# Performance work log

Measured on AMD Instinct MI355X. Metric: run time of the kernel, lower is better.

## Reference

```python
import jax, jax.numpy as jnp
import numpy as np

EPS = 1e-6
NUM_HEADS = 16


def _layernorm(x, g, b):
    m = jnp.mean(x, axis=-1, keepdims=True)
    v = jnp.mean(jnp.square(x - m), axis=-1, keepdims=True)
    return (x - m) / jnp.sqrt(v + EPS) * g + b


def _rotate_half(x):
    x1, x2 = jnp.split(x, 2, axis=-1)
    return jnp.concatenate([-x2, x1], axis=-1)


def setup_inputs() -> dict:
    key = jax.random.key(0)
    B, N, C = 2, 2048, 1024
    H = NUM_HEADS
    D = C // H
    F = int(C * 4.0)
    ks = jax.random.split(key, 12)
    s = 0.02
    pos = jnp.arange(N)[:, None].astype(jnp.float32)
    inv_freq = 1.0 / (10000.0 ** (jnp.arange(0, D, 2, dtype=jnp.float32) / D))
    freqs = pos * inv_freq[None, :]          # [N, D/2]
    emb = jnp.concatenate([freqs, freqs], axis=-1)  # [N, D]
    return {
        "x": jax.random.normal(ks[0], (B, N, C), jnp.float32),
        "rotary_cos": jnp.cos(emb),
        "rotary_sin": jnp.sin(emb),
        "ln1_g": jnp.ones((C,), jnp.float32),
        "ln1_b": jnp.zeros((C,), jnp.float32),
        "Wq": jax.random.normal(ks[1], (C, C), jnp.float32) * s,
        "bq": jnp.zeros((C,), jnp.float32),
        "Wk": jax.random.normal(ks[2], (C, C), jnp.float32) * s,
        "bk": jnp.zeros((C,), jnp.float32),
        "Wv": jax.random.normal(ks[3], (C, C), jnp.float32) * s,
        "bv": jnp.zeros((C,), jnp.float32),
        "Wo": jax.random.normal(ks[4], (C, C), jnp.float32) * s,
        "bo": jnp.zeros((C,), jnp.float32),
        "ln2_g": jnp.ones((C,), jnp.float32),
        "ln2_b": jnp.zeros((C,), jnp.float32),
        "W1": jax.random.normal(ks[5], (F, C), jnp.float32) * s,
        "b1": jnp.zeros((F,), jnp.float32),
        "W2": jax.random.normal(ks[6], (C, F), jnp.float32) * s,
        "b2": jnp.zeros((C,), jnp.float32),
    }


def reference(x, rotary_cos, rotary_sin, ln1_g, ln1_b, Wq, bq, Wk, bk, Wv, bv,
              Wo, bo, ln2_g, ln2_b, W1, b1, W2, b2):
    B, N, C = x.shape
    H = NUM_HEADS
    D = C // H

    # --- attention branch ---
    h = _layernorm(x, ln1_g, ln1_b)
    q = (h @ Wq.T + bq).reshape(B, N, H, D).transpose(0, 2, 1, 3)  # [B,H,N,D]
    k = (h @ Wk.T + bk).reshape(B, N, H, D).transpose(0, 2, 1, 3)
    v = (h @ Wv.T + bv).reshape(B, N, H, D).transpose(0, 2, 1, 3)

    cos = rotary_cos[None, None, :, :]  # [1,1,N,D]
    sin = rotary_sin[None, None, :, :]
    q = q * cos + _rotate_half(q) * sin
    k = k * cos + _rotate_half(k) * sin

    scale = D ** -0.5
    attn = jnp.einsum('bhnd,bhmd->bhnm', q, k) * scale
    attn = jax.nn.softmax(attn, axis=-1)
    out = jnp.einsum('bhnm,bhmd->bhnd', attn, v)
    out = out.transpose(0, 2, 1, 3).reshape(B, N, C)
    out = out @ Wo.T + bo
    x = x + out

    # --- MLP branch ---
    h = _layernorm(x, ln2_g, ln2_b)
    h = jax.nn.gelu(h @ W1.T + b1, approximate=False)  # torch nn.GELU exact
    h = h @ W2.T + b2
    return x + h
```

## Files before the change

### kernel.cpp

```cpp
#include <hip/hip_runtime.h>
#include <hip/hip_bf16.h>

#define B_ 2
#define N_ 2048
#define C_ 1024
#define H_ 16
#define D_ 64
#define F_ 4096
#define M_ 4096

typedef __attribute__((ext_vector_type(8))) short bf16x8;
typedef __attribute__((ext_vector_type(4))) float f32x4;

__device__ inline unsigned short f2bf(float f) {
  unsigned int u = __float_as_uint(f);
  u = (u + 0x7FFFu + ((u >> 16) & 1u)) >> 16;
  return (unsigned short)u;
}

__global__ __launch_bounds__(256)
void cvt_all(const float4* __restrict__ s0, const float4* __restrict__ s1,
             const float4* __restrict__ s2, const float4* __restrict__ s3,
             const float4* __restrict__ s4, const float4* __restrict__ s5,
             ushort4* __restrict__ d0, ushort4* __restrict__ d1,
             ushort4* __restrict__ d2, ushort4* __restrict__ d3,
             ushort4* __restrict__ d4, ushort4* __restrict__ d5) {
  int b = blockIdx.x;
  const float4* s; ushort4* d; int i;
  if      (b < 1024) { s = s0; d = d0; i = b * 256 + threadIdx.x; }
  else if (b < 2048) { s = s1; d = d1; i = (b - 1024) * 256 + threadIdx.x; }
  else if (b < 3072) { s = s2; d = d2; i = (b - 2048) * 256 + threadIdx.x; }
  else if (b < 4096) { s = s3; d = d3; i = (b - 3072) * 256 + threadIdx.x; }
  else if (b < 8192) { s = s4; d = d4; i = (b - 4096) * 256 + threadIdx.x; }
  else               { s = s5; d = d5; i = (b - 8192) * 256 + threadIdx.x; }
  float4 f = s[i];
  ushort4 o;
  o.x = f2bf(f.x); o.y = f2bf(f.y); o.z = f2bf(f.z); o.w = f2bf(f.w);
  d[i] = o;
}

__global__ __launch_bounds__(256)
void ln_kernel(const float* __restrict__ x, const float* __restrict__ g,
               const float* __restrict__ b, unsigned short* __restrict__ out) {
  __shared__ float red[8];
  const int row = blockIdx.x;
  const int t = threadIdx.x;
  const float4 xv = *(const float4*)(x + row * 1024 + t * 4);
  float s  = xv.x + xv.y + xv.z + xv.w;
  float sq = xv.x * xv.x + xv.y * xv.y + xv.z * xv.z + xv.w * xv.w;
  #pragma unroll
  for (int off = 32; off >= 1; off >>= 1) {
    s  += __shfl_down(s, off);
    sq += __shfl_down(sq, off);
  }
  const int lane = t & 63, wave = t >> 6;
  if (lane == 0) { red[wave * 2] = s; red[wave * 2 + 1] = sq; }
  __syncthreads();
  float ts = red[0] + red[2] + red[4] + red[6];
  float tq = red[1] + red[3] + red[5] + red[7];
  float mean = ts * (1.0f / 1024.0f);
  float var  = tq * (1.0f / 1024.0f) - mean * mean;
  float rstd = rsqrtf(var + 1e-6f);
  float xs[4] = {xv.x, xv.y, xv.z, xv.w};
  #pragma unroll
  for (int i = 0; i < 4; i++) {
    int c = t * 4 + i;
    float y = (xs[i] - mean) * rstd * g[c] + b[c];
    out[row * 1024 + c] = f2bf(y);
  }
}

template<int MODE, int BN>
__global__ __launch_bounds__(256)
void gemm_bt(const unsigned short* __restrict__ A,
             const unsigned short* __restrict__ Bw,
             int K, int Nout, int npc,
             const float* __restrict__ bias,
             const float* __restrict__ resid,
             unsigned short* __restrict__ out_bf,
             float* __restrict__ out_f32) {
  constexpr int NJ = BN / 32;
  __shared__ unsigned short sA[2][128 * 64];
  __shared__ unsigned short sB[2][BN * 64];
  const int t = threadIdx.x;
  const int wave = t >> 6, lane = t & 63;
  const int quad = lane >> 4, l16 = lane & 15;
  const int wm = (wave & 1) * 64, wn = (wave >> 1) * (BN / 2);
  const int id = blockIdx.y * gridDim.x + blockIdx.x;
  const int xcd = id & 7, r_ = id >> 3;
  const int m_blk = xcd * 4 + (r_ & 3);
  const int n_blk = r_ >> 2;
  const int m0 = m_blk * 128, n0 = n_blk * BN;

  f32x4 acc[4][NJ];
  #pragma unroll
  for (int i = 0; i < 4; i++)
    #pragma unroll
    for (int j = 0; j < NJ; j++) acc[i][j] = (f32x4){0.f, 0.f, 0.f, 0.f};

  const int sc = (((t & 7) ^ ((t >> 3) & 7)) * 8);
  const unsigned short* gA = A  + (m0 + (t >> 3)) * K + sc;
  const unsigned short* gB = Bw + (n0 + (t >> 3)) * K + sc;

  auto stage = [&](int k0, int buf) {
    unsigned short* lA = &sA[buf][(wave * 8) * 64];
    unsigned short* lB = &sB[buf][(wave * 8) * 64];
    #pragma unroll
    for (int i = 0; i < 4; i++)
      __builtin_amdgcn_global_load_lds((const unsigned int*)(gA + (32 * i) * K + k0),
                                       (unsigned int*)(lA + 32 * i * 64), 16, 0, 0);
    #pragma unroll
    for (int i = 0; i < BN / 32; i++)
      __builtin_amdgcn_global_load_lds((const unsigned int*)(gB + (32 * i) * K + k0),
                                       (unsigned int*)(lB + 32 * i * 64), 16, 0, 0);
  };

  stage(0, 0);
  __syncthreads();

  const int so0 = ((quad ^ (l16 & 7)) * 8);
  const int so1 = (((4 + quad) ^ (l16 & 7)) * 8);

  const int nk = K >> 6;
  for (int kt = 0; kt < nk; kt++) {
    const int cur = kt & 1;
    if (kt + 1 < nk) stage((kt + 1) * 64, cur ^ 1);
    #pragma unroll
    for (int kk = 0; kk < 2; kk++) {
      const int so = kk ? so1 : so0;
      bf16x8 af[4], bfr[NJ];
      #pragma unroll
      for (int i = 0; i < 4; i++)
        af[i] = *(const bf16x8*)(&sA[cur][(wm + i * 16 + l16) * 64 + so]);
      #pragma unroll
      for (int j = 0; j < NJ; j++)
        bfr[j] = *(const bf16x8*)(&sB[cur][(wn + j * 16 + l16) * 64 + so]);
      #pragma unroll
      for (int i = 0; i < 4; i++)
        #pragma unroll
        for (int j = 0; j < NJ; j++)
          acc[i][j] = __builtin_amdgcn_mfma_f32_16x16x32_bf16(af[i], bfr[j], acc[i][j], 0, 0, 0);
    }
    __syncthreads();
  }

  #pragma unroll
  for (int i = 0; i < 4; i++) {
    #pragma unroll
    for (int j = 0; j < NJ; j++) {
      int col = n0 + wn + j * 16 + l16;
      #pragma unroll
      for (int r = 0; r < 4; r++) {
        int row = m0 + wm + i * 16 + quad * 4 + r;
        float v = acc[i][j][r];
        if (MODE == 1 || MODE == 3) {
          out_f32[row * Nout + col] = v + bias[col] + resid[row * Nout + col];
        } else {
          v += bias[col];
          float w = v * (1.0f + 0.044715f * v * v);
          float gl = v / (1.0f + __expf(-1.5957691216f * w));
          out_bf[row * Nout + col] = f2bf(gl);
        }
      }
    }
  }
}

template<int EPI>
__global__ __launch_bounds__(512, 1)
void gemm256(const unsigned short* __restrict__ A,
             const unsigned short* __restrict__ Bw,
             const float* __restrict__ bias,
             const float* __restrict__ bq, const float* __restrict__ bk,
             const float* __restrict__ bv,
             const float* __restrict__ rc, const float* __restrict__ rs,
             unsigned short* __restrict__ o0,
             unsigned short* __restrict__ ko, unsigned short* __restrict__ vt) {
  const int K = 1024;
  __shared__ unsigned short sA[2][256 * 64];
  __shared__ unsigned short sB[2][256 * 64];
  const int t = threadIdx.x;
  const int wave = t >> 6, lane = t & 63;
  const int quad = lane >> 4, l16 = lane & 15;
  const int wm = (wave & 1) * 128, wn = (wave >> 1) * 64;
  const int id = blockIdx.x;
  const int xcd = id & 7, r_ = id >> 3;
  int m_blk, n_blk;
  if (EPI == 0) { n_blk = xcd * 2 + (r_ >> 4); m_blk = r_ & 15; }
  else          { m_blk = xcd * 2 + r_ / 12;   n_blk = r_ % 12; }
  const int m0 = m_blk * 256, n0 = n_blk * 256;

  f32x4 acc[8][4];
  #pragma unroll
  for (int i = 0; i < 8; i++)
    #pragma unroll
    for (int j = 0; j < 4; j++) acc[i][j] = (f32x4){0.f, 0.f, 0.f, 0.f};

  const int sc = (((t & 7) ^ ((t >> 3) & 7)) * 8);
  const unsigned short* gA = A  + (m0 + (t >> 3)) * K + sc;
  const unsigned short* gB = Bw + (n0 + (t >> 3)) * K + sc;

  auto stage_pair = [&](int k0, int buf, int pr) {
    if (pr < 2) {
      unsigned short* lA = &sA[buf][(wave * 8) * 64];
      #pragma unroll
      for (int r = pr * 2; r < pr * 2 + 2; r++)
        __builtin_amdgcn_global_load_lds((const unsigned int*)(gA + (64 * r) * K + k0),
                                         (unsigned int*)(lA + 64 * r * 64), 16, 0, 0);
    } else {
      unsigned short* lB = &sB[buf][(wave * 8) * 64];
      #pragma unroll
      for (int r = (pr - 2) * 2; r < (pr - 2) * 2 + 2; r++)
        __builtin_amdgcn_global_load_lds((const unsigned int*)(gB + (64 * r) * K + k0),
                                         (unsigned int*)(lB + 64 * r * 64), 16, 0, 0);
    }
  };

  stage_pair(0, 0, 0); stage_pair(0, 0, 1); stage_pair(0, 0, 2); stage_pair(0, 0, 3);
  stage_pair(64, 1, 0);
  asm volatile("s_waitcnt vmcnt(2)" ::: "memory");
  __builtin_amdgcn_s_barrier();

  const int so0 = ((quad ^ (l16 & 7)) * 8);
  const int so1 = (((4 + quad) ^ (l16 & 7)) * 8);

  const int nk = K >> 6;
  for (int t_ = 0; t_ < nk; t_++) {
    const int R = t_ & 1;
    const unsigned short* rA = sA[R];
    const unsigned short* rB = sB[R];
    #pragma unroll
    for (int p = 0; p < 4; p++) {
      const int kk = p >> 1, ih = p & 1;
      const int so = kk ? so1 : so0;
      bf16x8 af[4], bfr[4];
      #pragma unroll
      for (int ii = 0; ii < 4; ii++)
        af[ii] = *(const bf16x8*)(&rA[(wm + (ih * 4 + ii) * 16 + l16) * 64 + so]);
      #pragma unroll
      for (int j = 0; j < 4; j++)
        bfr[j] = *(const bf16x8*)(&rB[(wn + j * 16 + l16) * 64 + so]);
      if (p < 3 && t_ + 1 < nk) stage_pair((t_ + 1) * 64, R ^ 1, p + 1);
      __builtin_amdgcn_s_barrier();
      asm volatile("s_waitcnt lgkmcnt(0)" ::: "memory");
      __builtin_amdgcn_sched_barrier(0);
      __builtin_amdgcn_s_setprio(1);
      #pragma unroll
      for (int ii = 0; ii < 4; ii++)
        #pragma unroll
        for (int j = 0; j < 4; j++)
          acc[ih * 4 + ii][j] =
              __builtin_amdgcn_mfma_f32_16x16x32_bf16(af[ii], bfr[j], acc[ih * 4 + ii][j], 0, 0, 0);
      __builtin_amdgcn_s_setprio(0);
      if (p < 3) __builtin_amdgcn_s_barrier();
    }
    __builtin_amdgcn_s_barrier();
    if (t_ + 2 < nk) {
      stage_pair((t_ + 2) * 64, R, 0);
      asm volatile("s_waitcnt vmcnt(2)" ::: "memory");
      __builtin_amdgcn_s_barrier();
    } else if (t_ + 1 < nk) {
      asm volatile("s_waitcnt vmcnt(0)" ::: "memory");
      __builtin_amdgcn_s_barrier();
    }
  }

  if (EPI == 0) {
    #pragma unroll
    for (int i = 0; i < 8; i++) {
      #pragma unroll
      for (int j = 0; j < 4; j++) {
        int col = n0 + wn + j * 16 + l16;
        float bb = bias[col];
        #pragma unroll
        for (int r = 0; r < 4; r++) {
          int row = m0 + wm + i * 16 + quad * 4 + r;
          float v = acc[i][j][r] + bb;
          float w = v * (1.0f + 0.044715f * v * v);
          float gl = v / (1.0f + __expf(-1.5957691216f * w));
          o0[row * 4096 + col] = f2bf(gl);
        }
      }
    }
  } else {
    const int rgn = n_blk >> 2;
    const int c0 = (n_blk & 3) * 256;
    if (rgn == 2) {
      #pragma unroll
      for (int i = 0; i < 8; i++) {
        int row0 = m0 + wm + i * 16 + quad * 4;
        int bidx = row0 >> 11, n0r = row0 & 2047;
        #pragma unroll
        for (int j = 0; j < 4; j++) {
          int d = j * 16 + l16;
          int c = c0 + wn + d;
          int h = c >> 6;
          float bb = bv[c];
          __hip_bfloat162 p01 = __float22bfloat162_rn(float2{acc[i][j][0] + bb, acc[i][j][1] + bb});
          __hip_bfloat162 p23 = __float22bfloat162_rn(float2{acc[i][j][2] + bb, acc[i][j][3] + bb});
          unsigned int u01, u23;
          __builtin_memcpy(&u01, &p01, 4);
          __builtin_memcpy(&u23, &p23, 4);
          *(uint2*)(vt + (((bidx * 16 + h) * 64) + d) * 2048 + n0r) = make_uint2(u01, u23);
        }
      }
    } else {
      const float* bia = (rgn == 0) ? bq : bk;
      unsigned short* outp = (rgn == 0) ? o0 : ko;
      #pragma unroll
      for (int i = 0; i < 8; i++) {
        #pragma unroll
        for (int r = 0; r < 4; r++) {
          int row = m0 + wm + i * 16 + quad * 4 + r;
          int bidx = row >> 11, n = row & 2047;
          #pragma unroll
          for (int j = 0; j < 4; j++) {
            int d = j * 16 + l16;
            int c = c0 + wn + d;
            int h = c >> 6;
            int oi = ((bidx * 16 + h) * 2048 + n) * 64 + d;
            float val = acc[i][j][r] + bia[c];
            float pv  = acc[i][j ^ 2][r] + bia[c ^ 32];
            float rot = (j < 2) ? -pv : pv;
            float y = val * rc[n * 64 + d] + rot * rs[n * 64 + d];
            if (rgn == 0) y *= 0.125f;
            outp[oi] = f2bf(y);
          }
        }
      }
    }
  }
}

__global__ __launch_bounds__(256)
void flash_attn(const unsigned short* __restrict__ q,
                const unsigned short* __restrict__ k,
                const unsigned short* __restrict__ vt,
                unsigned short* __restrict__ o) {
  __shared__ unsigned short sK[2][64 * 64];
  __shared__ unsigned short sVt[2][64 * 64];
  __shared__ unsigned short sPt[2][4][16 * 72];
  const int t = threadIdx.x;
  const int wave = t >> 6, lane = t & 63;
  const int quad = lane >> 4, l16 = lane & 15;
  const int id = blockIdx.y * gridDim.x + blockIdx.x;
  const int bh = (id & 7) * 4 + ((id >> 3) & 3);
  const int qb = id >> 5;
  const int base = bh * (N_ * D_);

  bf16x8 qa[2][2];
  #pragma unroll
  for (int qt = 0; qt < 2; qt++) {
    int qrow = qb * 128 + wave * 32 + qt * 16 + l16;
    #pragma unroll
    for (int kk = 0; kk < 2; kk++)
      qa[qt][kk] = *(const bf16x8*)(q + base + qrow * D_ + kk * 32 + quad * 8);
  }
  float l_i[2] = {0.f, 0.f};
  f32x4 o_acc[2][4];
  #pragma unroll
  for (int qt = 0; qt < 2; qt++)
    #pragma unroll
    for (int dt = 0; dt < 4; dt++) o_acc[qt][dt] = (f32x4){0.f, 0.f, 0.f, 0.f};

  const int sc = (((t & 7) ^ ((t >> 3) & 7)) * 8);
  const unsigned short* gK  = k  + base + (t >> 3) * 64 + sc;
  const unsigned short* gVt = vt + bh * (64 * 2048) + (t >> 3) * 2048 + sc;

  auto stage = [&](int kt, int buf) {
    unsigned short* lK = &sK[buf][(wave * 8) * 64];
    unsigned short* lV = &sVt[buf][(wave * 8) * 64];
    #pragma unroll
    for (int i = 0; i < 2; i++) {
      __builtin_amdgcn_global_load_lds((const unsigned int*)(gK + (kt * 64 + 32 * i) * 64),
                                       (unsigned int*)(lK + 32 * i * 64), 16, 0, 0);
      __builtin_amdgcn_global_load_lds((const unsigned int*)(gVt + 32 * i * 2048 + kt * 64),
                                       (unsigned int*)(lV + 32 * i * 64), 16, 0, 0);
    }
  };
  stage(0, 0);
  __syncthreads();

  const int so0 = ((quad ^ (l16 & 7)) * 8);
  const int so1 = (((4 + quad) ^ (l16 & 7)) * 8);

  for (int kt = 0; kt < N_ / 64; kt++) {
    const int cur = kt & 1;
    if (kt < N_ / 64 - 1) stage(kt + 1, cur ^ 1);

    f32x4 s_acc[2][4];
    #pragma unroll
    for (int nt = 0; nt < 4; nt++) {
      bf16x8 kb0 = *(const bf16x8*)(&sK[cur][(nt * 16 + l16) * 64 + so0]);
      bf16x8 kb1 = *(const bf16x8*)(&sK[cur][(nt * 16 + l16) * 64 + so1]);
      #pragma unroll
      for (int qt = 0; qt < 2; qt++) {
        f32x4 a = (f32x4){0.f, 0.f, 0.f, 0.f};
        a = __builtin_amdgcn_mfma_f32_16x16x32_bf16(kb0, qa[qt][0], a, 0, 0, 0);
        a = __builtin_amdgcn_mfma_f32_16x16x32_bf16(kb1, qa[qt][1], a, 0, 0, 0);
        s_acc[qt][nt] = a;
      }
    }
    #pragma unroll
    for (int qt = 0; qt < 2; qt++) {
      float rsum = 0.f;
      #pragma unroll
      for (int nt = 0; nt < 4; nt++)
        #pragma unroll
        for (int r = 0; r < 4; r++) {
          float p = __expf(s_acc[qt][nt][r]);
          s_acc[qt][nt][r] = p;
          rsum += p;
        }
      rsum += __shfl_xor(rsum, 16);
      rsum += __shfl_xor(rsum, 32);
      l_i[qt] += rsum;
      #pragma unroll
      for (int nt = 0; nt < 4; nt++) {
        __hip_bfloat162 p01 = __float22bfloat162_rn(float2{s_acc[qt][nt][0], s_acc[qt][nt][1]});
        __hip_bfloat162 p23 = __float22bfloat162_rn(float2{s_acc[qt][nt][2], s_acc[qt][nt][3]});
        unsigned int u01, u23;
        __builtin_memcpy(&u01, &p01, 4);
        __builtin_memcpy(&u23, &p23, 4);
        *(uint2*)(&sPt[qt][wave][l16 * 72 + nt * 16 + quad * 4]) = make_uint2(u01, u23);
      }
    }
    __asm__ volatile("s_waitcnt lgkmcnt(0)" ::: "memory");
    bf16x8 pt[2][2];
    #pragma unroll
    for (int qt = 0; qt < 2; qt++) {
      pt[qt][0] = *(const bf16x8*)(&sPt[qt][wave][l16 * 72 + quad * 8]);
      pt[qt][1] = *(const bf16x8*)(&sPt[qt][wave][l16 * 72 + 32 + quad * 8]);
    }
    #pragma unroll
    for (int dt = 0; dt < 4; dt++) {
      int d0 = dt * 16 + l16;
      bf16x8 va0 = *(const bf16x8*)(&sVt[cur][d0 * 64 + so0]);
      bf16x8 va1 = *(const bf16x8*)(&sVt[cur][d0 * 64 + so1]);
      #pragma unroll
      for (int qt = 0; qt < 2; qt++) {
        o_acc[qt][dt] = __builtin_amdgcn_mfma_f32_16x16x32_bf16(va0, pt[qt][0], o_acc[qt][dt], 0, 0, 0);
        o_acc[qt][dt] = __builtin_amdgcn_mfma_f32_16x16x32_bf16(va1, pt[qt][1], o_acc[qt][dt], 0, 0, 0);
      }
    }
    __syncthreads();
  }

  const int b = bh >> 4, h = bh & 15;
  #pragma unroll
  for (int qt = 0; qt < 2; qt++) {
    const float inv = 1.0f / l_i[qt];
    const int tok = b * N_ + qb * 128 + wave * 32 + qt * 16 + l16;
    #pragma unroll
    for (int dt = 0; dt < 4; dt++) {
      __hip_bfloat162 p01 = __float22bfloat162_rn(float2{o_acc[qt][dt][0] * inv, o_acc[qt][dt][1] * inv});
      __hip_bfloat162 p23 = __float22bfloat162_rn(float2{o_acc[qt][dt][2] * inv, o_acc[qt][dt][3] * inv});
      unsigned int u01, u23;
      __builtin_memcpy(&u01, &p01, 4);
      __builtin_memcpy(&u23, &p23, 4);
      int col = h * 64 + dt * 16 + quad * 4;
      *(uint2*)(o + tok * C_ + col) = make_uint2(u01, u23);
    }
  }
}

extern "C" void kernel_launch(void* const* d_in, const int* in_sizes, int n_in,
                              void* d_out, int out_size, void* d_ws, size_t ws_size,
                              hipStream_t stream) {
  const float* x   = (const float*)d_in[0];
  const float* rc  = (const float*)d_in[1];
  const float* rs  = (const float*)d_in[2];
  const float* g1  = (const float*)d_in[3];
  const float* be1 = (const float*)d_in[4];
  const float* Wq  = (const float*)d_in[5];
  const float* bq  = (const float*)d_in[6];
  const float* Wk  = (const float*)d_in[7];
  const float* bk  = (const float*)d_in[8];
  const float* Wv  = (const float*)d_in[9];
  const float* bv  = (const float*)d_in[10];
  const float* Wo  = (const float*)d_in[11];
  const float* bo  = (const float*)d_in[12];
  const float* g2  = (const float*)d_in[13];
  const float* be2 = (const float*)d_in[14];
  const float* W1  = (const float*)d_in[15];
  const float* b1m = (const float*)d_in[16];
  const float* W2  = (const float*)d_in[17];
  const float* b2m = (const float*)d_in[18];
  float* out = (float*)d_out;

  char* ws = (char*)d_ws;
  unsigned short* wqkv = (unsigned short*)(ws + 0);
  unsigned short* wo   = (unsigned short*)(ws + 6291456);
  unsigned short* w1   = (unsigned short*)(ws + 8388608);
  unsigned short* w2   = (unsigned short*)(ws + 16777216);
  unsigned short* h1   = (unsigned short*)(ws + 25165824);
  unsigned short* qa   = (unsigned short*)(ws + 33554432);
  unsigned short* ka   = (unsigned short*)(ws + 41943040);
  unsigned short* va   = (unsigned short*)(ws + 50331648);
  unsigned short* ao   = (unsigned short*)(ws + 58720256);
  float*          x1   = (float*)(ws + 67108864);
  unsigned short* u    = (unsigned short*)(ws + 33554432);

  cvt_all<<<12288, 256, 0, stream>>>(
      (const float4*)Wq, (const float4*)Wk, (const float4*)Wv, (const float4*)Wo,
      (const float4*)W1, (const float4*)W2,
      (ushort4*)wqkv, (ushort4*)(wqkv + 1048576), (ushort4*)(wqkv + 2097152),
      (ushort4*)wo, (ushort4*)w1, (ushort4*)w2);

  ln_kernel<<<4096, 256, 0, stream>>>(x, g1, be1, h1);
  gemm256<1><<<192, 512, 0, stream>>>(h1, wqkv, nullptr, bq, bk, bv, rc, rs, qa, ka, va);
  flash_attn<<<dim3(16, 32), 256, 0, stream>>>(qa, ka, va, ao);
  gemm_bt<1, 64><<<dim3(16, 32), 256, 0, stream>>>(ao, wo, 1024, 1024, 2, bo, x, nullptr, x1);
  ln_kernel<<<4096, 256, 0, stream>>>(x1, g2, be2, h1);
  gemm256<0><<<256, 512, 0, stream>>>(h1, w1, b1m, nullptr, nullptr, nullptr, nullptr, nullptr,
                                      u, nullptr, nullptr);
  gemm_bt<3, 64><<<dim3(16, 32), 256, 0, stream>>>(u, w2, 4096, 1024, 2, b2m, x1, nullptr, out);
}
```

Baseline: 373.9 us.

## Split flash attention over KV halves with 512-thread blocks and a combine kernel

Flash attention now splits the key/value sequence into two halves, each handled by a separate block of 512 threads covering 256 query rows. Each block writes an unnormalized bf16 partial output and its row sums, and a new attn_norm kernel adds the halves and divides by the total sum. The aim is more parallelism and shorter per-block loops, at the cost of an extra kernel launch and extra partial-output traffic. Partials are rounded to bf16 before combining, which adds some rounding error. The merge is only exact because the softmax is apparently computed without a running max, so both halves share the same implicit scale.

Measured after the change: 375.6 us. Within noise of the previous version (+0.4%).

```diff
diff --git a/kernel.cpp b/kernel.cpp
--- a/kernel.cpp
+++ b/kernel.cpp
@@ -16,6 +16,10 @@
   unsigned int u = __float_as_uint(f);
   u = (u + 0x7FFFu + ((u >> 16) & 1u)) >> 16;
   return (unsigned short)u;
+}
+__device__ inline float bf2f(unsigned short u) {
+  unsigned int x = ((unsigned int)u) << 16;
+  return __uint_as_float(x);
 }
 
 __global__ __launch_bounds__(256)
@@ -332,26 +336,29 @@
   }
 }
 
-__global__ __launch_bounds__(256)
+__global__ __launch_bounds__(512)
 void flash_attn(const unsigned short* __restrict__ q,
                 const unsigned short* __restrict__ k,
                 const unsigned short* __restrict__ vt,
-                unsigned short* __restrict__ o) {
+                unsigned short* __restrict__ o0h,
+                unsigned short* __restrict__ o1h,
+                float* __restrict__ l0g, float* __restrict__ l1g) {
   __shared__ unsigned short sK[2][64 * 64];
   __shared__ unsigned short sVt[2][64 * 64];
-  __shared__ unsigned short sPt[2][4][16 * 72];
+  __shared__ unsigned short sPt[2][8][16 * 72];
   const int t = threadIdx.x;
   const int wave = t >> 6, lane = t & 63;
   const int quad = lane >> 4, l16 = lane & 15;
-  const int id = blockIdx.y * gridDim.x + blockIdx.x;
+  const int id = blockIdx.x;
   const int bh = (id & 7) * 4 + ((id >> 3) & 3);
-  const int qb = id >> 5;
+  const int qb = (id >> 5) & 7;
+  const int kvh = id >> 8;
   const int base = bh * (N_ * D_);
 
   bf16x8 qa[2][2];
   #pragma unroll
   for (int qt = 0; qt < 2; qt++) {
-    int qrow = qb * 128 + wave * 32 + qt * 16 + l16;
+    int qrow = qb * 256 + wave * 32 + qt * 16 + l16;
     #pragma unroll
     for (int kk = 0; kk < 2; kk++)
       qa[qt][kk] = *(const bf16x8*)(q + base + qrow * D_ + kk * 32 + quad * 8);
@@ -368,25 +375,21 @@
   const unsigned short* gVt = vt + bh * (64 * 2048) + (t >> 3) * 2048 + sc;
 
   auto stage = [&](int kt, int buf) {
-    unsigned short* lK = &sK[buf][(wave * 8) * 64];
-    unsigned short* lV = &sVt[buf][(wave * 8) * 64];
-    #pragma unroll
-    for (int i = 0; i < 2; i++) {
-      __builtin_amdgcn_global_load_lds((const unsigned int*)(gK + (kt * 64 + 32 * i) * 64),
-                                       (unsigned int*)(lK + 32 * i * 64), 16, 0, 0);
-      __builtin_amdgcn_global_load_lds((const unsigned int*)(gVt + 32 * i * 2048 + kt * 64),
-                                       (unsigned int*)(lV + 32 * i * 64), 16, 0, 0);
-    }
+    __builtin_amdgcn_global_load_lds((const unsigned int*)(gK + kt * 64 * 64),
+                                     (unsigned int*)(&sK[buf][(wave * 8) * 64]), 16, 0, 0);
+    __builtin_amdgcn_global_load_lds((const unsigned int*)(gVt + kt * 64),
+                                     (unsigned int*)(&sVt[buf][(wave * 8) * 64]), 16, 0, 0);
   };
-  stage(0, 0);
+  const int kt0 = kvh * 16, kt1 = kt0 + 16;
+  stage(kt0, 0);
   __syncthreads();
 
   const int so0 = ((quad ^ (l16 & 7)) * 8);
   const int so1 = (((4 + quad) ^ (l16 & 7)) * 8);
 
-  for (int kt = 0; kt < N_ / 64; kt++) {
+  for (int kt = kt0; kt < kt1; kt++) {
     const int cur = kt & 1;
-    if (kt < N_ / 64 - 1) stage(kt + 1, cur ^ 1);
+    if (kt + 1 < kt1) stage(kt + 1, cur ^ 1);
 
     f32x4 s_acc[2][4];
     #pragma unroll
@@ -446,22 +449,53 @@
     __syncthreads();
   }
 
+  unsigned short* op = kvh ? o1h : o0h;
+  float* lp = kvh ? l1g : l0g;
   const int b = bh >> 4, h = bh & 15;
   #pragma unroll
   for (int qt = 0; qt < 2; qt++) {
-    const float inv = 1.0f / l_i[qt];
-    const int tok = b * N_ + qb * 128 + wave * 32 + qt * 16 + l16;
+    const int qrow = qb * 256 + wave * 32 + qt * 16 + l16;
+    if (quad == 0) lp[bh * 2048 + qrow] = l_i[qt];
+    const int tok = b * N_ + qrow;
     #pragma unroll
     for (int dt = 0; dt < 4; dt++) {
-      __hip_bfloat162 p01 = __float22bfloat162_rn(float2{o_acc[qt][dt][0] * inv, o_acc[qt][dt][1] * inv});
-      __hip_bfloat162 p23 = __float22bfloat162_rn(float2{o_acc[qt][dt][2] * inv, o_acc[qt][dt][3] * inv});
+      __hip_bfloat162 p01 = __float22bfloat162_rn(float2{o_acc[qt][dt][0], o_acc[qt][dt][1]});
+      __hip_bfloat162 p23 = __float22bfloat162_rn(float2{o_acc[qt][dt][2], o_acc[qt][dt][3]});
       unsigned int u01, u23;
       __builtin_memcpy(&u01, &p01, 4);
       __builtin_memcpy(&u23, &p23, 4);
       int col = h * 64 + dt * 16 + quad * 4;
-      *(uint2*)(o + tok * C_ + col) = make_uint2(u01, u23);
-    }
-  }
+      *(uint2*)(op + tok * C_ + col) = make_uint2(u01, u23);
+    }
+  }
+}
+
+__global__ __launch_bounds__(256)
+void attn_norm(const unsigned short* __restrict__ o0h,
+               const unsigned short* __restrict__ o1h,
+               const float* __restrict__ l0g, const float* __restrict__ l1g,
+               unsigned short* __restrict__ o) {
+  const int i = (blockIdx.x * 256 + threadIdx.x) * 8;
+  const int row = i >> 10, c = i & 1023;
+  const int h = c >> 6;
+  const int b = row >> 11, n = row & 2047;
+  const int li = (b * 16 + h) * 2048 + n;
+  const float inv = 1.0f / (l0g[li] + l1g[li]);
+  ushort4 a0 = *(const ushort4*)(o0h + i);
+  ushort4 a1 = *(const ushort4*)(o0h + i + 4);
+  ushort4 b0 = *(const ushort4*)(o1h + i);
+  ushort4 b1 = *(const ushort4*)(o1h + i + 4);
+  ushort4 r0, r1;
+  r0.x = f2bf((bf2f(a0.x) + bf2f(b0.x)) * inv);
+  r0.y = f2bf((bf2f(a0.y) + bf2f(b0.y)) * inv);
+  r0.z = f2bf((bf2f(a0.z) + bf2f(b0.z)) * inv);
+  r0.w = f2bf((bf2f(a0.w) + bf2f(b0.w)) * inv);
+  r1.x = f2bf((bf2f(a1.x) + bf2f(b1.x)) * inv);
+  r1.y = f2bf((bf2f(a1.y) + bf2f(b1.y)) * inv);
+  r1.z = f2bf((bf2f(a1.z) + bf2f(b1.z)) * inv);
+  r1.w = f2bf((bf2f(a1.w) + bf2f(b1.w)) * inv);
+  *(ushort4*)(o + i) = r0;
+  *(ushort4*)(o + i + 4) = r1;
 }
 
 extern "C" void kernel_launch(void* const* d_in, const int* in_sizes, int n_in,
@@ -499,6 +533,8 @@
   unsigned short* va   = (unsigned short*)(ws + 50331648);
   unsigned short* ao   = (unsigned short*)(ws + 58720256);
   float*          x1   = (float*)(ws + 67108864);
+  float*          l0   = (float*)(ws + 67108864);
+  float*          l1   = l0 + 65536;
   unsigned short* u    = (unsigned short*)(ws + 33554432);
 
   cvt_all<<<12288, 256, 0, stream>>>(
@@ -509,7 +545,8 @@
 
   ln_kernel<<<4096, 256, 0, stream>>>(x, g1, be1, h1);
   gemm256<1><<<192, 512, 0, stream>>>(h1, wqkv, nullptr, bq, bk, bv, rc, rs, qa, ka, va);
-  flash_attn<<<dim3(16, 32), 256, 0, stream>>>(qa, ka, va, ao);
+  flash_attn<<<512, 512, 0, stream>>>(qa, ka, va, ao, h1, l0, l1);
+  attn_norm<<<2048, 256, 0, stream>>>(ao, h1, l0, l1, ao);
   gemm_bt<1, 64><<<dim3(16, 32), 256, 0, stream>>>(ao, wo, 1024, 1024, 2, bo, x, nullptr, x1);
   ln_kernel<<<4096, 256, 0, stream>>>(x1, g2, be2, h1);
   gemm256<0><<<256, 512, 0, stream>>>(h1, w1, b1m, nullptr, nullptr, nullptr, nullptr, nullptr,
```
